# Kernel optimization log

Hardware: AMD Instinct MI355X
Metric: run time of the kernel (lower is better)

Reference implementation:

```python
import jax, jax.numpy as jnp
import numpy as np

N, E = 50000, 800000
IN, HID, H, OUT = 128, 32, 4, 32
NEG_SLOPE = 0.2


def _gatv2_layer(x, edge_index, Wl, bl, Wr, br, att, bias, heads, ch, concat):
    """One GATv2Conv layer (PyG semantics: add self-loops, lin_l on source,
    lin_r on target, e = att . leaky_relu(gl_src + gr_dst), segment softmax
    over incoming edges of each target, scatter-add weighted source messages)."""
    n = x.shape[0]
    loop = jnp.arange(n)
    src = jnp.concatenate([edge_index[0], loop])
    dst = jnp.concatenate([edge_index[1], loop])

    gl = (x @ Wl + bl).reshape(n, heads, ch)   # source transform [N,H,C]
    gr = (x @ Wr + br).reshape(n, heads, ch)   # target transform [N,H,C]

    m = jax.nn.leaky_relu(gl[src] + gr[dst], NEG_SLOPE)   # [E+N,H,C]
    e = jnp.einsum('ehc,hc->eh', m, att)                   # [E+N,H]

    # numerically stable segment softmax over dst
    emax = jax.lax.stop_gradient(jax.ops.segment_max(e, dst, num_segments=n))
    ex = jnp.exp(e - emax[dst])
    denom = jax.ops.segment_sum(ex, dst, num_segments=n)
    alpha = ex / denom[dst]                                # [E+N,H]

    out = jax.ops.segment_sum(alpha[:, :, None] * gl[src], dst, num_segments=n)  # [N,H,C]
    out = out.reshape(n, heads * ch) if concat else out.mean(axis=1)
    return out + bias


def setup_inputs() -> dict:
    key = jax.random.key(0)
    ks = jax.random.split(key, 16)
    s = 0.05
    return {
        'x': jax.random.normal(ks[0], (N, IN), dtype=jnp.float32),
        'edge_index': jax.random.randint(ks[1], (2, E), 0, N, dtype=jnp.int32),
        # layer 1: IN -> HID, H heads, concat
        'Wl1': jax.random.normal(ks[2], (IN, H * HID), dtype=jnp.float32) * s,
        'bl1': jnp.zeros((H * HID,), dtype=jnp.float32),
        'Wr1': jax.random.normal(ks[3], (IN, H * HID), dtype=jnp.float32) * s,
        'br1': jnp.zeros((H * HID,), dtype=jnp.float32),
        'att1': jax.random.normal(ks[4], (H, HID), dtype=jnp.float32) * s,
        'bias1': jnp.zeros((H * HID,), dtype=jnp.float32),
        # layer 2: H*HID -> OUT, 1 head, no concat
        'Wl2': jax.random.normal(ks[5], (H * HID, OUT), dtype=jnp.float32) * s,
        'bl2': jnp.zeros((OUT,), dtype=jnp.float32),
        'Wr2': jax.random.normal(ks[6], (H * HID, OUT), dtype=jnp.float32) * s,
        'br2': jnp.zeros((OUT,), dtype=jnp.float32),
        'att2': jax.random.normal(ks[7], (1, OUT), dtype=jnp.float32) * s,
        'bias2': jnp.zeros((OUT,), dtype=jnp.float32),
    }


def reference(x, edge_index, Wl1, bl1, Wr1, br1, att1, bias1,
              Wl2, bl2, Wr2, br2, att2, bias2):
    h = jax.nn.elu(_gatv2_layer(x, edge_index, Wl1, bl1, Wr1, br1, att1, bias1, H, HID, True))
    # dropout inactive in eval mode
    return _gatv2_layer(h, edge_index, Wl2, bl2, Wr2, br2, att2, bias2, 1, OUT, False)
```

## Files before the change

### kernel.cpp

```cpp
#include <hip/hip_runtime.h>

#define NNODES 50000
#define NEDGES 800000
#define ETOT   (NNODES + NEDGES)
#define NEG 0.2f
#define BKTS 196
#define P1E 4096
#define NP1 ((ETOT + P1E - 1) / P1E)

typedef unsigned short ushort_t;
typedef unsigned int uint_t;
typedef __attribute__((ext_vector_type(8))) short short8;
typedef __attribute__((ext_vector_type(4))) float f32x4;

__device__ __forceinline__ ushort_t f2bf(float f) {
  uint_t u = __float_as_uint(f);
  u += 0x7FFFu + ((u >> 16) & 1u);
  return (ushort_t)(u >> 16);
}
__device__ __forceinline__ float bf2f(ushort_t h) {
  return __uint_as_float((uint_t)h << 16);
}

__global__ __launch_bounds__(256) void coarse_hist(const int* __restrict__ ei,
                                                   int* __restrict__ pcnt) {
  __shared__ int c[BKTS];
  for (int i = threadIdx.x; i < BKTS; i += 256) c[i] = 0;
  __syncthreads();
  int e0 = blockIdx.x * P1E;
#pragma unroll
  for (int t = 0; t < P1E / 256; ++t) {
    int i = e0 + t * 256 + (int)threadIdx.x;
    if (i < ETOT) {
      int dst = (i < NEDGES) ? ei[NEDGES + i] : (i - NEDGES);
      atomicAdd(&c[dst >> 8], 1);
    }
  }
  __syncthreads();
  for (int i = threadIdx.x; i < BKTS; i += 256)
    pcnt[blockIdx.x * BKTS + i] = c[i];
}

__global__ __launch_bounds__(256) void coarse_scan(const int* __restrict__ pcnt,
                                                   int* __restrict__ goffArr,
                                                   int* __restrict__ bucketStart,
                                                   int* __restrict__ rowptr) {
  __shared__ int tot[BKTS];
  int b = threadIdx.x;
  if (b < BKTS) {
    int run = 0;
    for (int k = 0; k < NP1; ++k) {
      goffArr[k * BKTS + b] = run;
      run += pcnt[k * BKTS + b];
    }
    tot[b] = run;
  }
  __syncthreads();
  if (threadIdx.x == 0) {
    int r = 0;
    for (int i = 0; i < BKTS; ++i) { bucketStart[i] = r; r += tot[i]; }
    bucketStart[BKTS] = r;
    rowptr[NNODES] = ETOT;
  }
}

__global__ __launch_bounds__(256) void bin_phase1(const int* __restrict__ ei,
                                                  const int* __restrict__ bucketStart,
                                                  const int* __restrict__ goffArr,
                                                  uint_t* __restrict__ binned) {
  __shared__ int cnt[BKTS], pref[BKTS], fillL[BKTS];
  __shared__ uint_t stage[P1E];
  int e0 = blockIdx.x * P1E;
  for (int i = threadIdx.x; i < BKTS; i += 256) { cnt[i] = 0; fillL[i] = 0; }
  __syncthreads();
  uint_t mypk[P1E / 256];
  int mybkt[P1E / 256];
#pragma unroll
  for (int t = 0; t < P1E / 256; ++t) {
    int i = e0 + t * 256 + (int)threadIdx.x;
    if (i < ETOT) {
      int dst = (i < NEDGES) ? ei[NEDGES + i] : (i - NEDGES);
      int src = (i < NEDGES) ? ei[i] : dst;
      int b = dst >> 8;
      mypk[t] = (uint_t)src | ((uint_t)(dst & 255) << 16) | ((uint_t)b << 24);
      mybkt[t] = b;
      atomicAdd(&cnt[b], 1);
    } else mybkt[t] = -1;
  }
  __syncthreads();
  if (threadIdx.x == 0) {
    int r = 0;
    for (int b = 0; b < BKTS; ++b) { pref[b] = r; r += cnt[b]; }
  }
  __syncthreads();
#pragma unroll
  for (int t = 0; t < P1E / 256; ++t) {
    if (mybkt[t] >= 0) {
      int p = pref[mybkt[t]] + atomicAdd(&fillL[mybkt[t]], 1);
      stage[p] = mypk[t];
    }
  }
  __syncthreads();
  int total = (e0 + P1E <= ETOT) ? P1E : (ETOT - e0);
  for (int j = threadIdx.x; j < total; j += 256) {
    uint_t pk = stage[j];
    int b = pk >> 24;
    binned[bucketStart[b] + goffArr[blockIdx.x * BKTS + b] + (j - pref[b])] = pk;
  }
}

__global__ __launch_bounds__(256) void bin_phase2(const uint_t* __restrict__ binned,
                                                  const int* __restrict__ bucketStart,
                                                  int* __restrict__ rowptr,
                                                  int* __restrict__ csrc) {
  __shared__ int cnt[256], pref[256], fillL[256];
  __shared__ int outS[8192];
  int b = blockIdx.x;
  int base = bucketStart[b];
  int cntAll = bucketStart[b + 1] - base;
  cnt[threadIdx.x] = 0; fillL[threadIdx.x] = 0;
  __syncthreads();
  for (int j = threadIdx.x; j < cntAll; j += 256)
    atomicAdd(&cnt[(binned[base + j] >> 16) & 255], 1);
  __syncthreads();
  if (threadIdx.x == 0) {
    int r = 0;
    for (int i = 0; i < 256; ++i) { pref[i] = r; r += cnt[i]; }
  }
  __syncthreads();
  int node = b * 256 + (int)threadIdx.x;
  if (node < NNODES) rowptr[node] = base + pref[threadIdx.x];
  for (int j = threadIdx.x; j < cntAll; j += 256) {
    uint_t pk = binned[base + j];
    int d = (pk >> 16) & 255;
    int p = pref[d] + atomicAdd(&fillL[d], 1);
    outS[p] = (int)(pk & 0xFFFF);
  }
  __syncthreads();
  for (int j = threadIdx.x; j < cntAll; j += 256)
    csrc[base + j] = outS[j];
}

__global__ __launch_bounds__(256) void prep_w(const float* __restrict__ Wl1,
                                              const float* __restrict__ Wr1,
                                              ushort_t* __restrict__ WtHi,
                                              ushort_t* __restrict__ WtLo) {
  int k = blockIdx.x;
  int n = threadIdx.x;
  float w = (n < 128) ? Wl1[k * 128 + n] : Wr1[k * 128 + (n - 128)];
  ushort_t h = f2bf(w);
  WtHi[n * 128 + k] = h;
  WtLo[n * 128 + k] = f2bf(w - bf2f(h));
}

__global__ __launch_bounds__(256) void gemm1_mfma(
    const float* __restrict__ x,
    const ushort_t* __restrict__ WtHi, const ushort_t* __restrict__ WtLo,
    const float* __restrict__ bl1, const float* __restrict__ br1,
    ushort_t* __restrict__ gl1, float* __restrict__ gr1) {
  constexpr int LDA = 132;
  __shared__ ushort_t Ahi[32][LDA];
  __shared__ ushort_t Alo[32][LDA];
  __shared__ float Cs[32][260];
  int m0 = blockIdx.x * 32;
  int tid = threadIdx.x;
#pragma unroll
  for (int i = 0; i < 4; ++i) {
    int it = i * 256 + tid;
    int row = it >> 5, c4 = it & 31;
    int gm = m0 + row;
    float4 v = (gm < NNODES) ? *(const float4*)&x[(size_t)gm * 128 + 4 * c4]
                             : make_float4(0.f, 0.f, 0.f, 0.f);
    ushort_t h0 = f2bf(v.x), h1 = f2bf(v.y), h2 = f2bf(v.z), h3 = f2bf(v.w);
    ushort_t l0 = f2bf(v.x - bf2f(h0)), l1 = f2bf(v.y - bf2f(h1));
    ushort_t l2 = f2bf(v.z - bf2f(h2)), l3 = f2bf(v.w - bf2f(h3));
    uint2 ph, pl;
    ph.x = (uint_t)h0 | ((uint_t)h1 << 16); ph.y = (uint_t)h2 | ((uint_t)h3 << 16);
    pl.x = (uint_t)l0 | ((uint_t)l1 << 16); pl.y = (uint_t)l2 | ((uint_t)l3 << 16);
    *(uint2*)&Ahi[row][4 * c4] = ph;
    *(uint2*)&Alo[row][4 * c4] = pl;
  }
  __syncthreads();
  int wave = tid >> 6, lane = tid & 63;
  int quad = lane >> 4, nl = lane & 15;
  int nb = wave * 64;
  f32x4 acc[2][4];
#pragma unroll
  for (int tm = 0; tm < 2; ++tm)
#pragma unroll
    for (int tn = 0; tn < 4; ++tn) acc[tm][tn] = (f32x4){0.f, 0.f, 0.f, 0.f};

#pragma unroll
  for (int kc = 0; kc < 4; ++kc) {
    int klane = kc * 32 + quad * 8;
    short8 ah[2], al[2], bh[4], bl[4];
#pragma unroll
    for (int tm = 0; tm < 2; ++tm) {
      ah[tm] = *(const short8*)&Ahi[16 * tm + nl][klane];
      al[tm] = *(const short8*)&Alo[16 * tm + nl][klane];
    }
#pragma unroll
    for (int tn = 0; tn < 4; ++tn) {
      size_t wo = (size_t)(nb + 16 * tn + nl) * 128 + klane;
      bh[tn] = *(const short8*)&WtHi[wo];
      bl[tn] = *(const short8*)&WtLo[wo];
    }
#pragma unroll
    for (int tm = 0; tm < 2; ++tm)
#pragma unroll
      for (int tn = 0; tn < 4; ++tn) {
        acc[tm][tn] = __builtin_amdgcn_mfma_f32_16x16x32_bf16(ah[tm], bh[tn], acc[tm][tn], 0, 0, 0);
        acc[tm][tn] = __builtin_amdgcn_mfma_f32_16x16x32_bf16(ah[tm], bl[tn], acc[tm][tn], 0, 0, 0);
        acc[tm][tn] = __builtin_amdgcn_mfma_f32_16x16x32_bf16(al[tm], bh[tn], acc[tm][tn], 0, 0, 0);
      }
  }
  float bb[4];
#pragma unroll
  for (int tn = 0; tn < 4; ++tn) {
    int n = nb + 16 * tn + nl;
    bb[tn] = (n < 128) ? bl1[n] : br1[n - 128];
  }
#pragma unroll
  for (int tm = 0; tm < 2; ++tm)
#pragma unroll
    for (int tn = 0; tn < 4; ++tn)
#pragma unroll
      for (int r = 0; r < 4; ++r)
        Cs[16 * tm + 4 * quad + r][nb + 16 * tn + nl] = acc[tm][tn][r] + bb[tn];
  __syncthreads();
#pragma unroll
  for (int i = 0; i < 2; ++i) {
    int it = i * 256 + tid;
    int row = it >> 4, oc = (it & 15) * 8;
    int gm = m0 + row;
    if (gm < NNODES) {
      uint4 pk;
      pk.x = (uint_t)f2bf(Cs[row][oc + 0]) | ((uint_t)f2bf(Cs[row][oc + 1]) << 16);
      pk.y = (uint_t)f2bf(Cs[row][oc + 2]) | ((uint_t)f2bf(Cs[row][oc + 3]) << 16);
      pk.z = (uint_t)f2bf(Cs[row][oc + 4]) | ((uint_t)f2bf(Cs[row][oc + 5]) << 16);
      pk.w = (uint_t)f2bf(Cs[row][oc + 6]) | ((uint_t)f2bf(Cs[row][oc + 7]) << 16);
      *(uint4*)&gl1[(size_t)gm * 128 + oc] = pk;
    }
  }
#pragma unroll
  for (int i = 0; i < 4; ++i) {
    int it = i * 256 + tid;
    int row = it >> 5, oc4 = (it & 31) * 4;
    int gm = m0 + row;
    if (gm < NNODES)
      *(float4*)&gr1[(size_t)gm * 128 + oc4] = *(const float4*)&Cs[row][128 + oc4];
  }
}

template<int BM, int BN, int MCOLS, bool BF16G1>
__global__ __launch_bounds__((BM / 8) * (BN / 8))
void gemm_tile(const float* __restrict__ A,
               const float* __restrict__ W1, const float* __restrict__ b1,
               const float* __restrict__ W2, const float* __restrict__ b2,
               void* __restrict__ G1v, float* __restrict__ G2) {
  constexpr int K = 128, KC = 32;
  constexpr int NT = (BM / 8) * (BN / 8);
  constexpr int LDA = BM + 4;
  __shared__ float AsT[KC][LDA];
  __shared__ float Ws[KC][BN];
  int row0 = blockIdx.x * BM;
  int n0   = blockIdx.y * BN;
  int tid = threadIdx.x;
  int tx = tid % (BN / 8), ty = tid / (BN / 8);
  float acc[8][8];
#pragma unroll
  for (int i = 0; i < 8; ++i)
#pragma unroll
    for (int j = 0; j < 8; ++j) acc[i][j] = 0.f;

  for (int kc = 0; kc < K; kc += KC) {
#pragma unroll
    for (int item = tid; item < BM * (KC / 4); item += NT) {
      int r = item >> 3, f4 = item & 7;
      int grow = row0 + r;
      float4 v = (grow < NNODES) ? *(const float4*)&A[(size_t)grow * K + kc + 4 * f4]
                                 : make_float4(0.f, 0.f, 0.f, 0.f);
      AsT[4 * f4 + 0][r] = v.x;
      AsT[4 * f4 + 1][r] = v.y;
      AsT[4 * f4 + 2][r] = v.z;
      AsT[4 * f4 + 3][r] = v.w;
    }
#pragma unroll
    for (int item = tid; item < KC * (BN / 4); item += NT) {
      int k = item / (BN / 4), c4 = item % (BN / 4);
      int ccat = n0 + 4 * c4;
      const float* src = (ccat < MCOLS)
          ? &W1[(size_t)(kc + k) * MCOLS + ccat]
          : &W2[(size_t)(kc + k) * MCOLS + ccat - MCOLS];
      *(float4*)&Ws[k][4 * c4] = *(const float4*)src;
    }
    __syncthreads();
#pragma unroll 8
    for (int k = 0; k < KC; ++k) {
      float4 a0 = *(const float4*)&AsT[k][4 * ty];
      float4 a1 = *(const float4*)&AsT[k][BM / 2 + 4 * ty];
      float4 w0 = *(const float4*)&Ws[k][4 * tx];
      float4 w1 = *(const float4*)&Ws[k][BN / 2 + 4 * tx];
      float av[8] = {a0.x, a0.y, a0.z, a0.w, a1.x, a1.y, a1.z, a1.w};
      float wv[8] = {w0.x, w0.y, w0.z, w0.w, w1.x, w1.y, w1.z, w1.w};
#pragma unroll
      for (int i = 0; i < 8; ++i)
#pragma unroll
        for (int j = 0; j < 8; ++j) acc[i][j] = fmaf(av[i], wv[j], acc[i][j]);
    }
    __syncthreads();
  }
#pragma unroll
  for (int i = 0; i < 8; ++i) {
    int row = row0 + (i < 4 ? 4 * ty + i : BM / 2 + 4 * ty + (i - 4));
    if (row >= NNODES) continue;
#pragma unroll
    for (int jj = 0; jj < 2; ++jj) {
      int ccat = n0 + (jj == 0 ? 4 * tx : BN / 2 + 4 * tx);
      float4 o = make_float4(acc[i][4 * jj + 0], acc[i][4 * jj + 1],
                             acc[i][4 * jj + 2], acc[i][4 * jj + 3]);
      if (ccat < MCOLS) {
        float4 bb = *(const float4*)&b1[ccat];
        o.x += bb.x; o.y += bb.y; o.z += bb.z; o.w += bb.w;
        if (BF16G1) {
          uint2 pk;
          pk.x = (uint_t)f2bf(o.x) | ((uint_t)f2bf(o.y) << 16);
          pk.y = (uint_t)f2bf(o.z) | ((uint_t)f2bf(o.w) << 16);
          *(uint2*)((ushort_t*)G1v + (size_t)row * MCOLS + ccat) = pk;
        } else {
          *(float4*)((float*)G1v + (size_t)row * MCOLS + ccat) = o;
        }
      } else {
        float4 bb = *(const float4*)&b2[ccat - MCOLS];
        o.x += bb.x; o.y += bb.y; o.z += bb.z; o.w += bb.w;
        *(float4*)&G2[(size_t)row * MCOLS + ccat - MCOLS] = o;
      }
    }
  }
}

__global__ __launch_bounds__(256) void gat1_edge(const int* __restrict__ rowptr,
                          const int* __restrict__ csrc,
                          const ushort_t* __restrict__ glb,
                          const float* __restrict__ gr,
                          const float* __restrict__ att, const float* __restrict__ bias,
                          float* __restrict__ hout) {
  int node = blockIdx.x * 4 + (threadIdx.x >> 6);
  if (node >= NNODES) return;
  int lane = threadIdx.x & 63;
  int eslot = lane >> 4;
  int q = lane & 15;
  int c8 = q * 8;
  float4 av0 = *(const float4*)(att + c8);
  float4 av1 = *(const float4*)(att + c8 + 4);
  float4 gr0 = *(const float4*)(gr + (size_t)node * 128 + c8);
  float4 gr1v = *(const float4*)(gr + (size_t)node * 128 + c8 + 4);
  int start = rowptr[node], end = rowptr[node + 1];
  float denom = 0.f;
  float4 A0 = make_float4(0.f, 0.f, 0.f, 0.f);
  float4 A1 = make_float4(0.f, 0.f, 0.f, 0.f);
  for (int b = start; b < end; b += 64) {
    int nb = end - b; if (nb > 64) nb = 64;
    int sidx = (lane < nb) ? csrc[b + lane] : 0;
    for (int j = 0; j < nb; j += 4) {
      bool pv = (j + eslot) < nb;
      int s = __shfl(sidx, j + eslot);
      uint4 up = *(const uint4*)(glb + (size_t)s * 128 + c8);
      float4 g0, g1;
      g0.x = __uint_as_float(up.x << 16);
      g0.y = __uint_as_float(up.x & 0xffff0000u);
      g0.z = __uint_as_float(up.y << 16);
      g0.w = __uint_as_float(up.y & 0xffff0000u);
      g1.x = __uint_as_float(up.z << 16);
      g1.y = __uint_as_float(up.z & 0xffff0000u);
      g1.z = __uint_as_float(up.w << 16);
      g1.w = __uint_as_float(up.w & 0xffff0000u);
      float t, v;
      t = g0.x + gr0.x; t = fmaxf(t, NEG * t); v = av0.x * t;
      t = g0.y + gr0.y; t = fmaxf(t, NEG * t); v = fmaf(av0.y, t, v);
      t = g0.z + gr0.z; t = fmaxf(t, NEG * t); v = fmaf(av0.z, t, v);
      t = g0.w + gr0.w; t = fmaxf(t, NEG * t); v = fmaf(av0.w, t, v);
      t = g1.x + gr1v.x; t = fmaxf(t, NEG * t); v = fmaf(av1.x, t, v);
      t = g1.y + gr1v.y; t = fmaxf(t, NEG * t); v = fmaf(av1.y, t, v);
      t = g1.z + gr1v.z; t = fmaxf(t, NEG * t); v = fmaf(av1.z, t, v);
      t = g1.w + gr1v.w; t = fmaxf(t, NEG * t); v = fmaf(av1.w, t, v);
      v += __shfl_xor(v, 1); v += __shfl_xor(v, 2);
      float ex = pv ? __expf(v) : 0.f;
      denom += ex;
      A0.x = fmaf(ex, g0.x, A0.x); A0.y = fmaf(ex, g0.y, A0.y);
      A0.z = fmaf(ex, g0.z, A0.z); A0.w = fmaf(ex, g0.w, A0.w);
      A1.x = fmaf(ex, g1.x, A1.x); A1.y = fmaf(ex, g1.y, A1.y);
      A1.z = fmaf(ex, g1.z, A1.z); A1.w = fmaf(ex, g1.w, A1.w);
    }
  }
  denom += __shfl_xor(denom, 16); denom += __shfl_xor(denom, 32);
  A0.x += __shfl_xor(A0.x, 16); A0.x += __shfl_xor(A0.x, 32);
  A0.y += __shfl_xor(A0.y, 16); A0.y += __shfl_xor(A0.y, 32);
  A0.z += __shfl_xor(A0.z, 16); A0.z += __shfl_xor(A0.z, 32);
  A0.w += __shfl_xor(A0.w, 16); A0.w += __shfl_xor(A0.w, 32);
  A1.x += __shfl_xor(A1.x, 16); A1.x += __shfl_xor(A1.x, 32);
  A1.y += __shfl_xor(A1.y, 16); A1.y += __shfl_xor(A1.y, 32);
  A1.z += __shfl_xor(A1.z, 16); A1.z += __shfl_xor(A1.z, 32);
  A1.w += __shfl_xor(A1.w, 16); A1.w += __shfl_xor(A1.w, 32);
  float inv = 1.f / denom;
  if (eslot == 0) {
    float4 bv = *(const float4*)(bias + c8);
    float4 o;
    o.x = A0.x * inv + bv.x; o.y = A0.y * inv + bv.y;
    o.z = A0.z * inv + bv.z; o.w = A0.w * inv + bv.w;
    o.x = o.x > 0.f ? o.x : __expf(o.x) - 1.f;
    o.y = o.y > 0.f ? o.y : __expf(o.y) - 1.f;
    o.z = o.z > 0.f ? o.z : __expf(o.z) - 1.f;
    o.w = o.w > 0.f ? o.w : __expf(o.w) - 1.f;
    *(float4*)(hout + (size_t)node * 128 + c8) = o;
  } else if (eslot == 1) {
    float4 bv = *(const float4*)(bias + c8 + 4);
    float4 o;
    o.x = A1.x * inv + bv.x; o.y = A1.y * inv + bv.y;
    o.z = A1.z * inv + bv.z; o.w = A1.w * inv + bv.w;
    o.x = o.x > 0.f ? o.x : __expf(o.x) - 1.f;
    o.y = o.y > 0.f ? o.y : __expf(o.y) - 1.f;
    o.z = o.z > 0.f ? o.z : __expf(o.z) - 1.f;
    o.w = o.w > 0.f ? o.w : __expf(o.w) - 1.f;
    *(float4*)(hout + (size_t)node * 128 + c8 + 4) = o;
  }
}

__global__ __launch_bounds__(256) void gat2_edge(const int* __restrict__ rowptr,
                          const int* __restrict__ csrc,
                          const float* __restrict__ gl, const float* __restrict__ gr,
                          const float* __restrict__ att, const float* __restrict__ bias,
                          float* __restrict__ out) {
  int node = blockIdx.x * 4 + (threadIdx.x >> 6);
  if (node >= NNODES) return;
  int lane = threadIdx.x & 63;
  int eslot = lane >> 3;
  int q = lane & 7;
  int c4 = q * 4;
  float4 avc = *(const float4*)(att + c4);
  float4 grd = *(const float4*)(gr + (size_t)node * 32 + c4);
  int start = rowptr[node], end = rowptr[node + 1];
  float denom = 0.f;
  float4 A = make_float4(0.f, 0.f, 0.f, 0.f);
  for (int b = start; b < end; b += 64) {
    int nb = end - b; if (nb > 64) nb = 64;
    int sidx = (lane < nb) ? csrc[b + lane] : 0;
    for (int j = 0; j < nb; j += 8) {
      bool pv = (j + eslot) < nb;
      int s = __shfl(sidx, j + eslot);
      float4 g = *(const float4*)(gl + (size_t)s * 32 + c4);
      float t, v;
      t = g.x + grd.x; t = fmaxf(t, NEG * t); v = avc.x * t;
      t = g.y + grd.y; t = fmaxf(t, NEG * t); v = fmaf(avc.y, t, v);
      t = g.z + grd.z; t = fmaxf(t, NEG * t); v = fmaf(avc.z, t, v);
      t = g.w + grd.w; t = fmaxf(t, NEG * t); v = fmaf(avc.w, t, v);
      v += __shfl_xor(v, 1); v += __shfl_xor(v, 2); v += __shfl_xor(v, 4);
      float ex = pv ? __expf(v) : 0.f;
      denom += ex;
      A.x = fmaf(ex, g.x, A.x); A.y = fmaf(ex, g.y, A.y);
      A.z = fmaf(ex, g.z, A.z); A.w = fmaf(ex, g.w, A.w);
    }
  }
  denom += __shfl_xor(denom, 8); denom += __shfl_xor(denom, 16); denom += __shfl_xor(denom, 32);
  A.x += __shfl_xor(A.x, 8); A.x += __shfl_xor(A.x, 16); A.x += __shfl_xor(A.x, 32);
  A.y += __shfl_xor(A.y, 8); A.y += __shfl_xor(A.y, 16); A.y += __shfl_xor(A.y, 32);
  A.z += __shfl_xor(A.z, 8); A.z += __shfl_xor(A.z, 16); A.z += __shfl_xor(A.z, 32);
  A.w += __shfl_xor(A.w, 8); A.w += __shfl_xor(A.w, 16); A.w += __shfl_xor(A.w, 32);
  if (eslot == 0) {
    float4 bv = *(const float4*)(bias + c4);
    float inv = 1.f / denom;
    float4 o;
    o.x = A.x * inv + bv.x; o.y = A.y * inv + bv.y;
    o.z = A.z * inv + bv.z; o.w = A.w * inv + bv.w;
    *(float4*)(out + (size_t)node * 32 + c4) = o;
  }
}

extern "C" void kernel_launch(void* const* d_in, const int* in_sizes, int n_in,
                              void* d_out, int out_size, void* d_ws, size_t ws_size,
                              hipStream_t stream) {
  const float* x     = (const float*)d_in[0];
  const int*   ei    = (const int*)  d_in[1];
  const float* Wl1   = (const float*)d_in[2];
  const float* bl1   = (const float*)d_in[3];
  const float* Wr1   = (const float*)d_in[4];
  const float* br1   = (const float*)d_in[5];
  const float* att1  = (const float*)d_in[6];
  const float* bias1 = (const float*)d_in[7];
  const float* Wl2   = (const float*)d_in[8];
  const float* bl2   = (const float*)d_in[9];
  const float* Wr2   = (const float*)d_in[10];
  const float* br2   = (const float*)d_in[11];
  const float* att2  = (const float*)d_in[12];
  const float* bias2 = (const float*)d_in[13];
  float* out = (float*)d_out;

  char* w = (char*)d_ws;
  auto carve = [&](size_t bytes) {
    char* p = w;
    w += (bytes + 255) & ~(size_t)255;
    return p;
  };
  ushort_t* gl1 = (ushort_t*)carve((size_t)NNODES * 128 * 2);
  float* gr1 = (float*)carve((size_t)NNODES * 128 * 4);
  float* h   = (float*)carve((size_t)NNODES * 128 * 4);
  float* gl2 = (float*)carve((size_t)NNODES * 32 * 4);
  float* gr2 = (float*)carve((size_t)NNODES * 32 * 4);
  ushort_t* WtHi = (ushort_t*)carve((size_t)256 * 128 * 2);
  ushort_t* WtLo = (ushort_t*)carve((size_t)256 * 128 * 2);
  int* pcnt    = (int*)carve((size_t)NP1 * BKTS * 4);
  int* goffArr = (int*)carve((size_t)NP1 * BKTS * 4);
  int* bucketStart = (int*)carve((size_t)(BKTS + 1) * 4);
  int* rowptr = (int*)carve((size_t)(NNODES + 1) * 4);
  uint_t* binned = (uint_t*)carve((size_t)ETOT * 4);
  int* csrc = (int*)carve((size_t)ETOT * 4);

  prep_w<<<128, 256, 0, stream>>>(Wl1, Wr1, WtHi, WtLo);
  coarse_hist<<<NP1, 256, 0, stream>>>(ei, pcnt);
  coarse_scan<<<1, 256, 0, stream>>>(pcnt, goffArr, bucketStart, rowptr);
  bin_phase1<<<NP1, 256, 0, stream>>>(ei, bucketStart, goffArr, binned);
  bin_phase2<<<BKTS, 256, 0, stream>>>(binned, bucketStart, rowptr, csrc);

  gemm1_mfma<<<(NNODES + 31) / 32, 256, 0, stream>>>(x, WtHi, WtLo, bl1, br1, gl1, gr1);
  gat1_edge<<<(NNODES + 3) / 4, 256, 0, stream>>>(rowptr, csrc, gl1, gr1, att1, bias1, h);
  gemm_tile<128, 64, 32, false><<<dim3((NNODES + 127) / 128, 1), 128, 0, stream>>>(
      h, Wl2, bl2, Wr2, br2, (void*)gl2, gr2);
  gat2_edge<<<(NNODES + 3) / 4, 256, 0, stream>>>(rowptr, csrc, gl2, gr2, att2, bias2, out);
}
```

Measured before the change: 275.8 us.

## Parallelize coarse bucket scan across blocks and prefetch CSR source indices in edge kernels

The single-block serial scan over per-partition bucket counts becomes one wavefront per bucket doing a shuffle-based prefix scan. The count and offset arrays are transposed to bucket-major so each scan reads contiguous memory, and a small second kernel computes bucket starts. Both GAT edge kernels now load the next chunk of 64 source indices before processing the current one, with a separate tail loop and partial unrolling. This targets the serialized scan latency and the index-load stall at each chunk boundary, at the cost of one extra kernel launch.

Result: no change. 278.8 us (+1.1%).

```diff
diff --git a/kernel.cpp b/kernel.cpp
--- a/kernel.cpp
+++ b/kernel.cpp
@@ -38,24 +38,32 @@
   }
   __syncthreads();
   for (int i = threadIdx.x; i < BKTS; i += 256)
-    pcnt[blockIdx.x * BKTS + i] = c[i];
-}
-
-__global__ __launch_bounds__(256) void coarse_scan(const int* __restrict__ pcnt,
-                                                   int* __restrict__ goffArr,
+    pcnt[i * NP1 + blockIdx.x] = c[i];
+}
+
+__global__ __launch_bounds__(64) void coarse_scan(const int* __restrict__ pcnt,
+                                                  int* __restrict__ goffArr,
+                                                  int* __restrict__ tot) {
+  int b = blockIdx.x;
+  int lane = threadIdx.x;
+  int carry = 0;
+  for (int k0 = 0; k0 < NP1; k0 += 64) {
+    int k = k0 + lane;
+    int v = (k < NP1) ? pcnt[b * NP1 + k] : 0;
+    int s = v;
+    for (int off = 1; off < 64; off <<= 1) {
+      int u = __shfl_up(s, off);
+      if (lane >= off) s += u;
+    }
+    if (k < NP1) goffArr[b * NP1 + k] = carry + s - v;
+    carry += __shfl(s, 63);
+  }
+  if (lane == 0) tot[b] = carry;
+}
+
+__global__ __launch_bounds__(256) void bucket_scan(const int* __restrict__ tot,
                                                    int* __restrict__ bucketStart,
                                                    int* __restrict__ rowptr) {
-  __shared__ int tot[BKTS];
-  int b = threadIdx.x;
-  if (b < BKTS) {
-    int run = 0;
-    for (int k = 0; k < NP1; ++k) {
-      goffArr[k * BKTS + b] = run;
-      run += pcnt[k * BKTS + b];
-    }
-    tot[b] = run;
-  }
-  __syncthreads();
   if (threadIdx.x == 0) {
     int r = 0;
     for (int i = 0; i < BKTS; ++i) { bucketStart[i] = r; r += tot[i]; }
@@ -105,7 +113,7 @@
   for (int j = threadIdx.x; j < total; j += 256) {
     uint_t pk = stage[j];
     int b = pk >> 24;
-    binned[bucketStart[b] + goffArr[blockIdx.x * BKTS + b] + (j - pref[b])] = pk;
+    binned[bucketStart[b] + goffArr[b * NP1 + blockIdx.x] + (j - pref[b])] = pk;
   }
 }
 
@@ -359,40 +367,49 @@
   float denom = 0.f;
   float4 A0 = make_float4(0.f, 0.f, 0.f, 0.f);
   float4 A1 = make_float4(0.f, 0.f, 0.f, 0.f);
-  for (int b = start; b < end; b += 64) {
-    int nb = end - b; if (nb > 64) nb = 64;
-    int sidx = (lane < nb) ? csrc[b + lane] : 0;
-    for (int j = 0; j < nb; j += 4) {
-      bool pv = (j + eslot) < nb;
-      int s = __shfl(sidx, j + eslot);
-      uint4 up = *(const uint4*)(glb + (size_t)s * 128 + c8);
-      float4 g0, g1;
-      g0.x = __uint_as_float(up.x << 16);
-      g0.y = __uint_as_float(up.x & 0xffff0000u);
-      g0.z = __uint_as_float(up.y << 16);
-      g0.w = __uint_as_float(up.y & 0xffff0000u);
-      g1.x = __uint_as_float(up.z << 16);
-      g1.y = __uint_as_float(up.z & 0xffff0000u);
-      g1.z = __uint_as_float(up.w << 16);
-      g1.w = __uint_as_float(up.w & 0xffff0000u);
-      float t, v;
-      t = g0.x + gr0.x; t = fmaxf(t, NEG * t); v = av0.x * t;
-      t = g0.y + gr0.y; t = fmaxf(t, NEG * t); v = fmaf(av0.y, t, v);
-      t = g0.z + gr0.z; t = fmaxf(t, NEG * t); v = fmaf(av0.z, t, v);
-      t = g0.w + gr0.w; t = fmaxf(t, NEG * t); v = fmaf(av0.w, t, v);
-      t = g1.x + gr1v.x; t = fmaxf(t, NEG * t); v = fmaf(av1.x, t, v);
-      t = g1.y + gr1v.y; t = fmaxf(t, NEG * t); v = fmaf(av1.y, t, v);
-      t = g1.z + gr1v.z; t = fmaxf(t, NEG * t); v = fmaf(av1.z, t, v);
-      t = g1.w + gr1v.w; t = fmaxf(t, NEG * t); v = fmaf(av1.w, t, v);
-      v += __shfl_xor(v, 1); v += __shfl_xor(v, 2);
-      float ex = pv ? __expf(v) : 0.f;
-      denom += ex;
-      A0.x = fmaf(ex, g0.x, A0.x); A0.y = fmaf(ex, g0.y, A0.y);
-      A0.z = fmaf(ex, g0.z, A0.z); A0.w = fmaf(ex, g0.w, A0.w);
-      A1.x = fmaf(ex, g1.x, A1.x); A1.y = fmaf(ex, g1.y, A1.y);
-      A1.z = fmaf(ex, g1.z, A1.z); A1.w = fmaf(ex, g1.w, A1.w);
-    }
-  }
+
+  auto body = [&](int s, bool pv) {
+    uint4 up = *(const uint4*)(glb + (size_t)s * 128 + c8);
+    float4 g0, g1;
+    g0.x = __uint_as_float(up.x << 16);
+    g0.y = __uint_as_float(up.x & 0xffff0000u);
+    g0.z = __uint_as_float(up.y << 16);
+    g0.w = __uint_as_float(up.y & 0xffff0000u);
+    g1.x = __uint_as_float(up.z << 16);
+    g1.y = __uint_as_float(up.z & 0xffff0000u);
+    g1.z = __uint_as_float(up.w << 16);
+    g1.w = __uint_as_float(up.w & 0xffff0000u);
+    float t, v;
+    t = g0.x + gr0.x; t = fmaxf(t, NEG * t); v = av0.x * t;
+    t = g0.y + gr0.y; t = fmaxf(t, NEG * t); v = fmaf(av0.y, t, v);
+    t = g0.z + gr0.z; t = fmaxf(t, NEG * t); v = fmaf(av0.z, t, v);
+    t = g0.w + gr0.w; t = fmaxf(t, NEG * t); v = fmaf(av0.w, t, v);
+    t = g1.x + gr1v.x; t = fmaxf(t, NEG * t); v = fmaf(av1.x, t, v);
+    t = g1.y + gr1v.y; t = fmaxf(t, NEG * t); v = fmaf(av1.y, t, v);
+    t = g1.z + gr1v.z; t = fmaxf(t, NEG * t); v = fmaf(av1.z, t, v);
+    t = g1.w + gr1v.w; t = fmaxf(t, NEG * t); v = fmaf(av1.w, t, v);
+    v += __shfl_xor(v, 1); v += __shfl_xor(v, 2);
+    float ex = pv ? __expf(v) : 0.f;
+    denom += ex;
+    A0.x = fmaf(ex, g0.x, A0.x); A0.y = fmaf(ex, g0.y, A0.y);
+    A0.z = fmaf(ex, g0.z, A0.z); A0.w = fmaf(ex, g0.w, A0.w);
+    A1.x = fmaf(ex, g1.x, A1.x); A1.y = fmaf(ex, g1.y, A1.y);
+    A1.z = fmaf(ex, g1.z, A1.z); A1.w = fmaf(ex, g1.w, A1.w);
+  };
+
+  int b = start;
+  int sidx = (b + lane < end) ? csrc[b + lane] : 0;
+  for (; b + 64 <= end; b += 64) {
+    int sn = (b + 64 + lane < end) ? csrc[b + 64 + lane] : 0;
+#pragma unroll 2
+    for (int j = 0; j < 64; j += 4)
+      body(__shfl(sidx, j + eslot), true);
+    sidx = sn;
+  }
+  int nb = end - b;
+  for (int j = 0; j < nb; j += 4)
+    body(__shfl(sidx, j + eslot), (j + eslot) < nb);
+
   denom += __shfl_xor(denom, 16); denom += __shfl_xor(denom, 32);
   A0.x += __shfl_xor(A0.x, 16); A0.x += __shfl_xor(A0.x, 32);
   A0.y += __shfl_xor(A0.y, 16); A0.y += __shfl_xor(A0.y, 32);
@@ -442,25 +459,34 @@
   int start = rowptr[node], end = rowptr[node + 1];
   float denom = 0.f;
   float4 A = make_float4(0.f, 0.f, 0.f, 0.f);
-  for (int b = start; b < end; b += 64) {
-    int nb = end - b; if (nb > 64) nb = 64;
-    int sidx = (lane < nb) ? csrc[b + lane] : 0;
-    for (int j = 0; j < nb; j += 8) {
-      bool pv = (j + eslot) < nb;
-      int s = __shfl(sidx, j + eslot);
-      float4 g = *(const float4*)(gl + (size_t)s * 32 + c4);
-      float t, v;
-      t = g.x + grd.x; t = fmaxf(t, NEG * t); v = avc.x * t;
-      t = g.y + grd.y; t = fmaxf(t, NEG * t); v = fmaf(avc.y, t, v);
-      t = g.z + grd.z; t = fmaxf(t, NEG * t); v = fmaf(avc.z, t, v);
-      t = g.w + grd.w; t = fmaxf(t, NEG * t); v = fmaf(avc.w, t, v);
-      v += __shfl_xor(v, 1); v += __shfl_xor(v, 2); v += __shfl_xor(v, 4);
-      float ex = pv ? __expf(v) : 0.f;
-      denom += ex;
-      A.x = fmaf(ex, g.x, A.x); A.y = fmaf(ex, g.y, A.y);
-      A.z = fmaf(ex, g.z, A.z); A.w = fmaf(ex, g.w, A.w);
-    }
-  }
+
+  auto body = [&](int s, bool pv) {
+    float4 g = *(const float4*)(gl + (size_t)s * 32 + c4);
+    float t, v;
+    t = g.x + grd.x; t = fmaxf(t, NEG * t); v = avc.x * t;
+    t = g.y + grd.y; t = fmaxf(t, NEG * t); v = fmaf(avc.y, t, v);
+    t = g.z + grd.z; t = fmaxf(t, NEG * t); v = fmaf(avc.z, t, v);
+    t = g.w + grd.w; t = fmaxf(t, NEG * t); v = fmaf(avc.w, t, v);
+    v += __shfl_xor(v, 1); v += __shfl_xor(v, 2); v += __shfl_xor(v, 4);
+    float ex = pv ? __expf(v) : 0.f;
+    denom += ex;
+    A.x = fmaf(ex, g.x, A.x); A.y = fmaf(ex, g.y, A.y);
+    A.z = fmaf(ex, g.z, A.z); A.w = fmaf(ex, g.w, A.w);
+  };
+
+  int b = start;
+  int sidx = (b + lane < end) ? csrc[b + lane] : 0;
+  for (; b + 64 <= end; b += 64) {
+    int sn = (b + 64 + lane < end) ? csrc[b + 64 + lane] : 0;
+#pragma unroll 2
+    for (int j = 0; j < 64; j += 8)
+      body(__shfl(sidx, j + eslot), true);
+    sidx = sn;
+  }
+  int nb = end - b;
+  for (int j = 0; j < nb; j += 8)
+    body(__shfl(sidx, j + eslot), (j + eslot) < nb);
+
   denom += __shfl_xor(denom, 8); denom += __shfl_xor(denom, 16); denom += __shfl_xor(denom, 32);
   A.x += __shfl_xor(A.x, 8); A.x += __shfl_xor(A.x, 16); A.x += __shfl_xor(A.x, 32);
   A.y += __shfl_xor(A.y, 8); A.y += __shfl_xor(A.y, 16); A.y += __shfl_xor(A.y, 32);
@@ -510,6 +536,7 @@
   ushort_t* WtLo = (ushort_t*)carve((size_t)256 * 128 * 2);
   int* pcnt    = (int*)carve((size_t)NP1 * BKTS * 4);
   int* goffArr = (int*)carve((size_t)NP1 * BKTS * 4);
+  int* tot     = (int*)carve((size_t)BKTS * 4);
   int* bucketStart = (int*)carve((size_t)(BKTS + 1) * 4);
   int* rowptr = (int*)carve((size_t)(NNODES + 1) * 4);
   uint_t* binned = (uint_t*)carve((size_t)ETOT * 4);
@@ -517,7 +544,8 @@
 
   prep_w<<<128, 256, 0, stream>>>(Wl1, Wr1, WtHi, WtLo);
   coarse_hist<<<NP1, 256, 0, stream>>>(ei, pcnt);
-  coarse_scan<<<1, 256, 0, stream>>>(pcnt, goffArr, bucketStart, rowptr);
+  coarse_scan<<<BKTS, 64, 0, stream>>>(pcnt, goffArr, tot);
+  bucket_scan<<<1, 256, 0, stream>>>(tot, bucketStart, rowptr);
   bin_phase1<<<NP1, 256, 0, stream>>>(ei, bucketStart, goffArr, binned);
   bin_phase2<<<BKTS, 256, 0, stream>>>(binned, bucketStart, rowptr, csrc);
 
```

## Parallelize coarse bucket scan across blocks and alias GEMM shared memory

Applied to the files above, without the earlier changes.

The single-block serial scan over partition counts (one thread per bucket looping over ~208 partitions) is replaced by one wavefront per bucket doing a shuffle-based prefix scan over a transposed pcnt layout, followed by a tiny bucket-level scan kernel. This removes a latency-bound serial kernel from the CSR build at the cost of one extra launch. Separately, gemm1_mfma now aliases its A staging buffers with the output staging buffer in shared memory, adding a barrier, to reduce LDS footprint and raise occupancy.

After: 272.7 us. No clear change (-1.1%).

```diff
diff --git a/kernel.cpp b/kernel.cpp
--- a/kernel.cpp
+++ b/kernel.cpp
@@ -38,24 +38,32 @@
   }
   __syncthreads();
   for (int i = threadIdx.x; i < BKTS; i += 256)
-    pcnt[blockIdx.x * BKTS + i] = c[i];
-}
-
-__global__ __launch_bounds__(256) void coarse_scan(const int* __restrict__ pcnt,
-                                                   int* __restrict__ goffArr,
+    pcnt[i * NP1 + blockIdx.x] = c[i];
+}
+
+__global__ __launch_bounds__(64) void coarse_scan(const int* __restrict__ pcnt,
+                                                  int* __restrict__ goffArr,
+                                                  int* __restrict__ tot) {
+  int b = blockIdx.x;
+  int lane = threadIdx.x;
+  int carry = 0;
+  for (int k0 = 0; k0 < NP1; k0 += 64) {
+    int k = k0 + lane;
+    int v = (k < NP1) ? pcnt[b * NP1 + k] : 0;
+    int s = v;
+    for (int off = 1; off < 64; off <<= 1) {
+      int u = __shfl_up(s, off);
+      if (lane >= off) s += u;
+    }
+    if (k < NP1) goffArr[b * NP1 + k] = carry + s - v;
+    carry += __shfl(s, 63);
+  }
+  if (lane == 0) tot[b] = carry;
+}
+
+__global__ __launch_bounds__(256) void bucket_scan(const int* __restrict__ tot,
                                                    int* __restrict__ bucketStart,
                                                    int* __restrict__ rowptr) {
-  __shared__ int tot[BKTS];
-  int b = threadIdx.x;
-  if (b < BKTS) {
-    int run = 0;
-    for (int k = 0; k < NP1; ++k) {
-      goffArr[k * BKTS + b] = run;
-      run += pcnt[k * BKTS + b];
-    }
-    tot[b] = run;
-  }
-  __syncthreads();
   if (threadIdx.x == 0) {
     int r = 0;
     for (int i = 0; i < BKTS; ++i) { bucketStart[i] = r; r += tot[i]; }
@@ -105,7 +113,7 @@
   for (int j = threadIdx.x; j < total; j += 256) {
     uint_t pk = stage[j];
     int b = pk >> 24;
-    binned[bucketStart[b] + goffArr[blockIdx.x * BKTS + b] + (j - pref[b])] = pk;
+    binned[bucketStart[b] + goffArr[b * NP1 + blockIdx.x] + (j - pref[b])] = pk;
   }
 }
 
@@ -159,9 +167,10 @@
     const float* __restrict__ bl1, const float* __restrict__ br1,
     ushort_t* __restrict__ gl1, float* __restrict__ gr1) {
   constexpr int LDA = 132;
-  __shared__ ushort_t Ahi[32][LDA];
-  __shared__ ushort_t Alo[32][LDA];
-  __shared__ float Cs[32][260];
+  __shared__ __align__(16) char smem[32 * 260 * 4];
+  ushort_t (*Ahi)[LDA] = (ushort_t(*)[LDA])smem;
+  ushort_t (*Alo)[LDA] = (ushort_t(*)[LDA])(smem + 32 * LDA * 2);
+  float (*Cs)[260] = (float(*)[260])smem;
   int m0 = blockIdx.x * 32;
   int tid = threadIdx.x;
 #pragma unroll
@@ -220,6 +229,7 @@
     int n = nb + 16 * tn + nl;
     bb[tn] = (n < 128) ? bl1[n] : br1[n - 128];
   }
+  __syncthreads();
 #pragma unroll
   for (int tm = 0; tm < 2; ++tm)
 #pragma unroll
@@ -510,6 +520,7 @@
   ushort_t* WtLo = (ushort_t*)carve((size_t)256 * 128 * 2);
   int* pcnt    = (int*)carve((size_t)NP1 * BKTS * 4);
   int* goffArr = (int*)carve((size_t)NP1 * BKTS * 4);
+  int* tot     = (int*)carve((size_t)BKTS * 4);
   int* bucketStart = (int*)carve((size_t)(BKTS + 1) * 4);
   int* rowptr = (int*)carve((size_t)(NNODES + 1) * 4);
   uint_t* binned = (uint_t*)carve((size_t)ETOT * 4);
@@ -517,7 +528,8 @@
 
   prep_w<<<128, 256, 0, stream>>>(Wl1, Wr1, WtHi, WtLo);
   coarse_hist<<<NP1, 256, 0, stream>>>(ei, pcnt);
-  coarse_scan<<<1, 256, 0, stream>>>(pcnt, goffArr, bucketStart, rowptr);
+  coarse_scan<<<BKTS, 64, 0, stream>>>(pcnt, goffArr, tot);
+  bucket_scan<<<1, 256, 0, stream>>>(tot, bucketStart, rowptr);
   bin_phase1<<<NP1, 256, 0, stream>>>(ei, bucketStart, goffArr, binned);
   bin_phase2<<<BKTS, 256, 0, stream>>>(binned, bucketStart, rowptr, csrc);
 
```
